# Optimization experiments

Hardware: AMD Instinct MI355X
Metric: run time of the kernel (lower is better)

## Reference

```python
import jax, jax.numpy as jnp
import numpy as np

H = 8          # num_heads
NEG = -1e30    # masked-score value
EPS = 1e-5


def layer_norm(h, g, b):
    mu = jnp.mean(h, -1, keepdims=True)
    v = jnp.mean(jnp.square(h - mu), -1, keepdims=True)
    return (h - mu) * jax.lax.rsqrt(v + EPS) * g + b


def mha(q_in, kv_in, in_w, in_b, out_w, out_b, mask):
    # in_w: [3D, D] packed q/k/v projections (PyTorch MultiheadAttention layout)
    D = q_in.shape[-1]
    dh = D // H
    wq, wk, wv = in_w[:D], in_w[D:2 * D], in_w[2 * D:]
    bq, bk, bv = in_b[:D], in_b[D:2 * D], in_b[2 * D:]
    q = (q_in @ wq.T + bq).reshape(q_in.shape[0], q_in.shape[1], H, dh)
    k = (kv_in @ wk.T + bk).reshape(kv_in.shape[0], kv_in.shape[1], H, dh)
    v = (kv_in @ wv.T + bv).reshape(kv_in.shape[0], kv_in.shape[1], H, dh)
    s = jnp.einsum('bqhd,bkhd->bhqk', q, k) / jnp.sqrt(jnp.float32(dh))
    if mask is not None:
        s = s + mask  # [1,1,S,S] additive causal mask
    a = jax.nn.softmax(s, axis=-1)
    o = jnp.einsum('bhqk,bkhd->bqhd', a, v).reshape(q_in.shape[0], q_in.shape[1], D)
    return o @ out_w.T + out_b


def _forward(x, start_query, one_emb, zero_emb,
             sa_in_w, sa_in_b, sa_out_w, sa_out_b,
             ca_in_w, ca_in_b, ca_out_w, ca_out_b,
             lin1_w, lin1_b, lin2_w, lin2_b,
             ln_g, ln_b, cls_w, cls_b, label):
    B, S, D = x.shape
    n = label.shape[0]  # == S
    # Teacher-forced decoder inputs: [start_query, emb(label[0]), ..., emb(label[n-2])]
    tok = jnp.where((label[:-1] > 0.5)[:, None], one_emb[None, :], zero_emb[None, :])  # [n-1, D]
    tgt = jnp.concatenate([start_query[None, :], tok], axis=0)  # [n, D]
    h = jnp.broadcast_to(tgt[None], (B, n, D))
    causal = jnp.tril(jnp.ones((n, n), dtype=bool))
    mask = jnp.where(causal, 0.0, NEG).astype(x.dtype)[None, None]
    L = sa_in_w.shape[0]
    for l in range(L):
        # post-LN TransformerDecoderLayer (PyTorch default, relu FFN)
        sa = mha(h, h, sa_in_w[l], sa_in_b[l], sa_out_w[l], sa_out_b[l], mask)
        h = layer_norm(h + sa, ln_g[l, 0], ln_b[l, 0])
        ca = mha(h, x, ca_in_w[l], ca_in_b[l], ca_out_w[l], ca_out_b[l], None)
        h = layer_norm(h + ca, ln_g[l, 1], ln_b[l, 1])
        ff = jax.nn.relu(h @ lin1_w[l].T + lin1_b[l]) @ lin2_w[l].T + lin2_b[l]
        h = layer_norm(h + ff, ln_g[l, 2], ln_b[l, 2])
    # classifier + sigmoid; output[b, i] == decoder(tf[:1+i])[-1] of the original loop
    return jax.nn.sigmoid(h @ cls_w.T + cls_b)  # [B, n, 1]


def setup_inputs() -> dict:
    key = jax.random.key(0)
    ks = iter(jax.random.split(key, 32))
    B, S, D, FF, L = 8, 1024, 1024, 2048, 6

    def w(shape, s=0.02):
        return jax.random.normal(next(ks), shape, jnp.float32) * s

    return dict(
        x=jax.random.normal(next(ks), (B, S, D), jnp.float32),
        label=jax.random.uniform(next(ks), (S,), jnp.float32),
        start_query=jax.random.uniform(next(ks), (D,), jnp.float32),
        one_emb=jax.random.uniform(next(ks), (D,), jnp.float32),
        zero_emb=jax.random.uniform(next(ks), (D,), jnp.float32),
        sa_in_w=w((L, 3 * D, D)), sa_in_b=jnp.zeros((L, 3 * D), jnp.float32),
        sa_out_w=w((L, D, D)), sa_out_b=jnp.zeros((L, D), jnp.float32),
        ca_in_w=w((L, 3 * D, D)), ca_in_b=jnp.zeros((L, 3 * D), jnp.float32),
        ca_out_w=w((L, D, D)), ca_out_b=jnp.zeros((L, D), jnp.float32),
        lin1_w=w((L, FF, D)), lin1_b=jnp.zeros((L, FF), jnp.float32),
        lin2_w=w((L, D, FF)), lin2_b=jnp.zeros((L, D), jnp.float32),
        ln_g=jnp.ones((L, 3, D), jnp.float32), ln_b=jnp.zeros((L, 3, D), jnp.float32),
        cls_w=w((1, D)), cls_b=jnp.zeros((1,), jnp.float32),
    )


def reference(x, label, start_query, one_emb, zero_emb,
              sa_in_w, sa_in_b, sa_out_w, sa_out_b,
              ca_in_w, ca_in_b, ca_out_w, ca_out_b,
              lin1_w, lin1_b, lin2_w, lin2_b,
              ln_g, ln_b, cls_w, cls_b):
    return _forward(x, start_query, one_emb, zero_emb,
                    sa_in_w, sa_in_b, sa_out_w, sa_out_b,
                    ca_in_w, ca_in_b, ca_out_w, ca_out_b,
                    lin1_w, lin1_b, lin2_w, lin2_b,
                    ln_g, ln_b, cls_w, cls_b, label)
```

## Files before the change

kernel.cpp:

```cpp
#include <hip/hip_runtime.h>
#include <stdint.h>

typedef __attribute__((ext_vector_type(8))) short short8;
typedef __attribute__((ext_vector_type(4))) float f32x4;
typedef __attribute__((ext_vector_type(4))) float float4v;
typedef __attribute__((ext_vector_type(4))) unsigned short ushort4v;

__device__ __forceinline__ float b2f(short u) {
  union { float f; uint32_t i; } v; v.i = ((uint32_t)(unsigned short)u) << 16; return v.f;
}
__device__ __forceinline__ short f2b(float f) {
  uint32_t x = __float_as_uint(f);
  uint32_t r = (x + 0x7fffu + ((x >> 16) & 1u)) >> 16;
  return (short)r;
}
__device__ __forceinline__ void gload16(const short* g, short* l) {
  __builtin_amdgcn_global_load_lds((__attribute__((address_space(1))) const void*)g,
                                   (__attribute__((address_space(3))) void*)l, 16, 0, 0);
}

__global__ void f2b_kernel(const float* __restrict__ in, short* __restrict__ out, int n4) {
  int i = blockIdx.x * blockDim.x + threadIdx.x;
  int stride = gridDim.x * blockDim.x;
  for (; i < n4; i += stride) {
    float4v v = *((const float4v*)in + i);
    ushort4v o;
    o[0] = (unsigned short)f2b(v[0]); o[1] = (unsigned short)f2b(v[1]);
    o[2] = (unsigned short)f2b(v[2]); o[3] = (unsigned short)f2b(v[3]);
    *((ushort4v*)out + i) = o;
  }
}

__global__ void h0_kernel(const float* __restrict__ label, const float* __restrict__ sq,
                          const float* __restrict__ onee, const float* __restrict__ zeroe,
                          short* __restrict__ h) {
  int i = blockIdx.x;
  const float* src = (i == 0) ? sq : (label[i - 1] > 0.5f ? onee : zeroe);
  int d = threadIdx.x * 4;
  float4v v = *(const float4v*)(src + d);
  ushort4v o;
  o[0] = (unsigned short)f2b(v[0]); o[1] = (unsigned short)f2b(v[1]);
  o[2] = (unsigned short)f2b(v[2]); o[3] = (unsigned short)f2b(v[3]);
#pragma unroll
  for (int b = 0; b < 8; ++b)
    *(ushort4v*)(h + ((size_t)b * 1024 + i) * 1024 + d) = o;
}

__device__ __forceinline__ void stage_grp(const short* __restrict__ mat, size_t rc0,
                                          int K, int kt, short* dstbuf, int w, int lane, int g2) {
  const int w3 = w & 3;
  const int rlo = lane >> 3;
  const int us = (lane & 7) ^ rlo;
#pragma unroll
  for (int q = 0; q < 4; ++q) {
    int c;
    if (w < 4) c = g2 * 8 + w3 * 2 + (q & 1) + (q >> 1) * 16;
    else       c = g2 * 4 + w3 + (q & 1) * 8 + (q >> 1) * 16;
    int rih = (c & 15) * 8 + rlo;
    gload16(mat + (rc0 + (c >> 4) * 128 + rih) * (size_t)K + kt * 64 + us * 8,
            dstbuf + ((w >> 2) * 32 + c) * 512);
  }
}

template <int EPI>
__global__ __launch_bounds__(512, 2) void gemm256(const short* __restrict__ A,
                                                  const short* __restrict__ W,
                                                  const float* __restrict__ bias,
                                                  short* __restrict__ C,
                                                  int M, int N, int K) {
  __shared__ short lds[2 * 4 * 8192];
  const int tid = threadIdx.x, lane = tid & 63, w = tid >> 6;
  const int g = lane >> 4, l15 = lane & 15;
  const int wm = w >> 2, wn = w & 3;
  const int nbx = N >> 8;
  int nwg = gridDim.x, orig = blockIdx.x, cpx = nwg >> 3;
  int id = (orig & 7) * cpx + (orig >> 3);
  int bx = id % nbx, by = id / nbx;
  const size_t rowA = (size_t)by * 256, colB = (size_t)bx * 256;
  const int NT = K >> 6;

  const short* smat = (w < 4) ? A : W;
  const size_t src0 = (w < 4) ? rowA : colB;

  f32x4 acc[8][4];
#pragma unroll
  for (int i = 0; i < 8; ++i)
#pragma unroll
    for (int j = 0; j < 4; ++j) acc[i][j] = (f32x4){0.f, 0.f, 0.f, 0.f};

  int sxz0 = g ^ (l15 & 7);
  int sxz1 = (4 + g) ^ (l15 & 7);
  const short* abase = lds + wm * 8192 + l15 * 64;
  const short* bbase = lds + (2 + (wn >> 1)) * 8192 + ((wn & 1) * 64 + l15) * 64;

  stage_grp(smat, src0, K, 0, lds, w, lane, 0);
  stage_grp(smat, src0, K, 0, lds, w, lane, 1);
  asm volatile("s_waitcnt vmcnt(0)" ::: "memory");
  __builtin_amdgcn_s_barrier();

  int p = 0;
  for (int t = 0; t < NT; ++t) {
    const int po = p * 32768;
    short* nbuf = lds + (p ^ 1) * 32768;
    if (t + 1 < NT) stage_grp(smat, src0, K, t + 1, nbuf, w, lane, 0);
    short8 af[4][2], bf0[2][2], bf1[2][2];

#pragma unroll
    for (int i = 0; i < 4; ++i) {
      af[i][0] = *(const short8*)(abase + po + i * 1024 + sxz0 * 8);
      af[i][1] = *(const short8*)(abase + po + i * 1024 + sxz1 * 8);
    }
#pragma unroll
    for (int j = 0; j < 2; ++j) {
      bf0[j][0] = *(const short8*)(bbase + po + j * 1024 + sxz0 * 8);
      bf0[j][1] = *(const short8*)(bbase + po + j * 1024 + sxz1 * 8);
    }
    __builtin_amdgcn_s_barrier();
    __builtin_amdgcn_s_setprio(1);
#pragma unroll
    for (int i = 0; i < 4; ++i)
#pragma unroll
      for (int j = 0; j < 2; ++j)
#pragma unroll
        for (int ks = 0; ks < 2; ++ks)
          acc[i][j] = __builtin_amdgcn_mfma_f32_16x16x32_bf16(af[i][ks], bf0[j][ks], acc[i][j], 0, 0, 0);
    __builtin_amdgcn_s_setprio(0);
    if (t + 1 < NT) {
      asm volatile("s_waitcnt vmcnt(4)" ::: "memory");
      stage_grp(smat, src0, K, t + 1, nbuf, w, lane, 1);
    } else {
      asm volatile("s_waitcnt vmcnt(0)" ::: "memory");
    }
    __builtin_amdgcn_s_barrier();

#pragma unroll
    for (int j = 0; j < 2; ++j) {
      bf1[j][0] = *(const short8*)(bbase + po + (2 + j) * 1024 + sxz0 * 8);
      bf1[j][1] = *(const short8*)(bbase + po + (2 + j) * 1024 + sxz1 * 8);
    }
    __builtin_amdgcn_s_barrier();
    __builtin_amdgcn_s_setprio(1);
#pragma unroll
    for (int i = 0; i < 4; ++i)
#pragma unroll
      for (int j = 0; j < 2; ++j)
#pragma unroll
        for (int ks = 0; ks < 2; ++ks)
          acc[i][2 + j] = __builtin_amdgcn_mfma_f32_16x16x32_bf16(af[i][ks], bf1[j][ks], acc[i][2 + j], 0, 0, 0);
    __builtin_amdgcn_s_setprio(0);
    __builtin_amdgcn_s_barrier();

#pragma unroll
    for (int i = 0; i < 4; ++i) {
      af[i][0] = *(const short8*)(abase + po + (64 + i * 16) * 64 + sxz0 * 8);
      af[i][1] = *(const short8*)(abase + po + (64 + i * 16) * 64 + sxz1 * 8);
    }
    __builtin_amdgcn_s_barrier();
    __builtin_amdgcn_s_setprio(1);
#pragma unroll
    for (int i = 0; i < 4; ++i)
#pragma unroll
      for (int j = 0; j < 2; ++j)
#pragma unroll
        for (int ks = 0; ks < 2; ++ks)
          acc[4 + i][2 + j] = __builtin_amdgcn_mfma_f32_16x16x32_bf16(af[i][ks], bf1[j][ks], acc[4 + i][2 + j], 0, 0, 0);
    __builtin_amdgcn_s_setprio(0);
    __builtin_amdgcn_s_barrier();

    __builtin_amdgcn_s_setprio(1);
#pragma unroll
    for (int i = 0; i < 4; ++i)
#pragma unroll
      for (int j = 0; j < 2; ++j)
#pragma unroll
        for (int ks = 0; ks < 2; ++ks)
          acc[4 + i][j] = __builtin_amdgcn_mfma_f32_16x16x32_bf16(af[i][ks], bf0[j][ks], acc[4 + i][j], 0, 0, 0);
    __builtin_amdgcn_s_setprio(0);

    asm volatile("s_waitcnt vmcnt(4)" ::: "memory");
    __builtin_amdgcn_s_barrier();
    p ^= 1;
  }

  float bv[4];
#pragma unroll
  for (int j = 0; j < 4; ++j) bv[j] = bias[colB + wn * 64 + j * 16 + l15];
#pragma unroll
  for (int i = 0; i < 8; ++i) {
    size_t row = rowA + wm * 128 + i * 16 + g * 4;
#pragma unroll
    for (int j = 0; j < 4; ++j) {
      size_t col = colB + wn * 64 + j * 16 + l15;
#pragma unroll
      for (int r = 0; r < 4; ++r) {
        float v = acc[i][j][r] + bv[j];
        if (EPI == 1) v = fmaxf(v, 0.f);
        C[(row + r) * N + col] = f2b(v);
      }
    }
  }
}

__device__ __forceinline__ void stage128(const short* __restrict__ A, const short* __restrict__ W,
                                         size_t rowA, size_t colB, int K, int kt,
                                         short* dstbuf, int w, int lane, int grp) {
  const int rlo = lane >> 3;
  const int us = (lane & 7) ^ rlo;
  const int coff = kt * 64 + us * 8;
  if (grp == 0) {
#pragma unroll
    for (int q = 0; q < 4; ++q) {
      int c = w * 4 + q;
      gload16(A + (rowA + c * 8 + rlo) * (size_t)K + coff, dstbuf + c * 512 + lane * 8);
    }
#pragma unroll
    for (int e = 0; e < 2; ++e) {
      int i8 = w * 2 + e;
      int bc = (i8 & 3) + ((i8 >> 2) << 3);
      gload16(W + (colB + bc * 8 + rlo) * (size_t)K + coff, dstbuf + 8192 + bc * 512 + lane * 8);
    }
  } else {
#pragma unroll
    for (int e = 0; e < 2; ++e) {
      int i8 = w * 2 + e;
      int bc = (i8 & 3) + 4 + ((i8 >> 2) << 3);
      gload16(W + (colB + bc * 8 + rlo) * (size_t)K + coff, dstbuf + 8192 + bc * 512 + lane * 8);
    }
  }
}

template <int EPI>
__global__ __launch_bounds__(256, 2) void gemm128(const short* __restrict__ A,
                                                  const short* __restrict__ W,
                                                  const float* __restrict__ bias,
                                                  short* __restrict__ C,
                                                  int M, int N, int K) {
  __shared__ short lds[2 * 16384];
  const int tid = threadIdx.x, lane = tid & 63, w = tid >> 6;
  const int g = lane >> 4, l15 = lane & 15;
  const int wm = w >> 1, wn = w & 1;
  const int nbx = N >> 7;
  int nwg = gridDim.x, orig = blockIdx.x, cpx = nwg >> 3;
  int id = (orig & 7) * cpx + (orig >> 3);
  int bx = id % nbx, by = id / nbx;
  const size_t rowA = (size_t)by * 128, colB = (size_t)bx * 128;
  const int NT = K >> 6;

  f32x4 acc[4][4];
#pragma unroll
  for (int i = 0; i < 4; ++i)
#pragma unroll
    for (int j = 0; j < 4; ++j) acc[i][j] = (f32x4){0.f, 0.f, 0.f, 0.f};

  const int sxz0 = g ^ (l15 & 7), sxz1 = (4 + g) ^ (l15 & 7);

  stage128(A, W, rowA, colB, K, 0, lds, w, lane, 0);
  stage128(A, W, rowA, colB, K, 0, lds, w, lane, 1);
  asm volatile("s_waitcnt vmcnt(0)" ::: "memory");
  __builtin_amdgcn_s_barrier();

  int p = 0;
  for (int t = 0; t < NT; ++t) {
    short* nbuf = lds + (p ^ 1) * 16384;
    if (t + 1 < NT) stage128(A, W, rowA, colB, K, t + 1, nbuf, w, lane, 0);
    const int po = p * 16384;
    short8 af[4][2], bf[2][2];
#pragma unroll
    for (int i = 0; i < 4; ++i) {
      int ra = wm * 64 + i * 16 + l15;
      af[i][0] = *(const short8*)(lds + po + ra * 64 + sxz0 * 8);
      af[i][1] = *(const short8*)(lds + po + ra * 64 + sxz1 * 8);
    }
#pragma unroll
    for (int j = 0; j < 2; ++j) {
      int rb = wn * 64 + j * 16 + l15;
      bf[j][0] = *(const short8*)(lds + po + 8192 + rb * 64 + sxz0 * 8);
      bf[j][1] = *(const short8*)(lds + po + 8192 + rb * 64 + sxz1 * 8);
    }
    __builtin_amdgcn_s_setprio(1);
#pragma unroll
    for (int i = 0; i < 4; ++i)
#pragma unroll
      for (int j = 0; j < 2; ++j)
#pragma unroll
        for (int ks = 0; ks < 2; ++ks)
          acc[i][j] = __builtin_amdgcn_mfma_f32_16x16x32_bf16(af[i][ks], bf[j][ks], acc[i][j], 0, 0, 0);
    __builtin_amdgcn_s_setprio(0);
    if (t + 1 < NT) {
      asm volatile("s_waitcnt vmcnt(6)" ::: "memory");
      stage128(A, W, rowA, colB, K, t + 1, nbuf, w, lane, 1);
    } else {
      asm volatile("s_waitcnt vmcnt(0)" ::: "memory");
    }
    __builtin_amdgcn_s_barrier();
#pragma unroll
    for (int j = 0; j < 2; ++j) {
      int rb = wn * 64 + 32 + j * 16 + l15;
      bf[j][0] = *(const short8*)(lds + po + 8192 + rb * 64 + sxz0 * 8);
      bf[j][1] = *(const short8*)(lds + po + 8192 + rb * 64 + sxz1 * 8);
    }
    __builtin_amdgcn_s_setprio(1);
#pragma unroll
    for (int i = 0; i < 4; ++i)
#pragma unroll
      for (int j = 0; j < 2; ++j)
#pragma unroll
        for (int ks = 0; ks < 2; ++ks)
          acc[i][2 + j] = __builtin_amdgcn_mfma_f32_16x16x32_bf16(af[i][ks], bf[j][ks], acc[i][2 + j], 0, 0, 0);
    __builtin_amdgcn_s_setprio(0);
    asm volatile("s_waitcnt vmcnt(2)" ::: "memory");
    __builtin_amdgcn_s_barrier();
    p ^= 1;
  }

  float bv[4];
#pragma unroll
  for (int j = 0; j < 4; ++j) bv[j] = bias[colB + wn * 64 + j * 16 + l15];
#pragma unroll
  for (int i = 0; i < 4; ++i) {
    size_t row = rowA + wm * 64 + i * 16 + g * 4;
#pragma unroll
    for (int j = 0; j < 4; ++j) {
      size_t col = colB + wn * 64 + j * 16 + l15;
#pragma unroll
      for (int r = 0; r < 4; ++r) {
        float v = acc[i][j][r] + bv[j];
        if (EPI == 1) v = fmaxf(v, 0.f);
        C[(row + r) * N + col] = f2b(v);
      }
    }
  }
}

__global__ __launch_bounds__(256) void tv_kernel(const short* __restrict__ src, int ld, int voff,
                                                 short* __restrict__ vt) {
  __shared__ short t[64 * 72];
  const int kt = blockIdx.x * 64, dt = blockIdx.y * 64, bh = blockIdx.z;
  const int b = bh >> 3, hh = bh & 7;
  const short* s = src + (size_t)(b * 1024 + kt) * ld + voff + hh * 128 + dt;
#pragma unroll
  for (int p = 0; p < 2; ++p) {
    int idx = p * 256 + threadIdx.x;
    int r = idx >> 3, u = idx & 7;
    *(short8*)&t[r * 72 + u * 8] = *(const short8*)&s[(size_t)r * ld + u * 8];
  }
  __syncthreads();
#pragma unroll
  for (int p = 0; p < 2; ++p) {
    int idx = p * 256 + threadIdx.x;
    int dd = idx >> 3, u = idx & 7;
    short8 o;
#pragma unroll
    for (int j = 0; j < 8; ++j) o[j] = t[(u * 8 + j) * 72 + dd];
    *(short8*)&vt[((size_t)bh * 128 + dt + dd) * 1024 + kt + u * 8] = o;
  }
}

template <bool CAUSAL>
__global__ __launch_bounds__(256, 2) void attn_kernel(const short* __restrict__ Qb, int ldq, int qoff,
                                                      const short* __restrict__ Kb, int ldk, int koff,
                                                      const short* __restrict__ Vt,
                                                      short* __restrict__ Ob) {
  __shared__ short k_lds[64 * 128];
  __shared__ short v_lds[128 * 64];
  __shared__ short p_lds[4 * 32 * 72];
  const int tid = threadIdx.x, lane = tid & 63, w = tid >> 6;
  const int g = lane >> 4, l15 = lane & 15;
  const int bh = blockIdx.x, b = bh >> 3, hh = bh & 7;
  const int qi = blockIdx.y;
  const int q0 = qi * 128;
  const float scale = 0.08838834764831845f;
  const int ntiles = CAUSAL ? (q0 >> 6) + 2 : 16;

  const int kr = w * 16 + (lane >> 4);
  const int vd = w * 32 + (lane >> 3);

  short8 qf[2][4];
#pragma unroll
  for (int fm = 0; fm < 2; ++fm) {
    int row = q0 + w * 32 + fm * 16 + l15;
    const short* qp = Qb + (size_t)(b * 1024 + row) * ldq + qoff + hh * 128;
#pragma unroll
    for (int t = 0; t < 4; ++t) qf[fm][t] = *(const short8*)(qp + t * 32 + g * 8);
  }

  f32x4 oacc[2][8];
  f32x4 lacc[2];
  float m_st[2][4];
#pragma unroll
  for (int fm = 0; fm < 2; ++fm) {
#pragma unroll
    for (int fo = 0; fo < 8; ++fo) oacc[fm][fo] = (f32x4){0.f, 0.f, 0.f, 0.f};
    lacc[fm] = (f32x4){0.f, 0.f, 0.f, 0.f};
#pragma unroll
    for (int r = 0; r < 4; ++r) m_st[fm][r] = -3.0e38f;
  }
  const short8 ones = {16256, 16256, 16256, 16256, 16256, 16256, 16256, 16256};

#pragma unroll
  for (int c = 0; c < 4; ++c) {
    int ch = w * 4 + c;
    int r = kr + c * 4;
    int us = (lane & 15) ^ (r & 7);
    gload16(Kb + (size_t)(b * 1024 + r) * ldk + koff + hh * 128 + us * 8, k_lds + ch * 512);
    int d = vd + c * 8;
    int usv = (lane & 7) ^ (d & 7);
    gload16(Vt + ((size_t)bh * 128 + d) * 1024 + usv * 8, v_lds + ch * 512);
  }
  __builtin_amdgcn_sched_barrier(0);
  short8 kreg[4], vreg[4];
  if (ntiles > 1) {
#pragma unroll
    for (int c = 0; c < 4; ++c) {
      int r = kr + c * 4;
      int us = (lane & 15) ^ (r & 7);
      kreg[c] = *(const short8*)(Kb + (size_t)(b * 1024 + 64 + r) * ldk + koff + hh * 128 + us * 8);
      int d = vd + c * 8;
      int usv = (lane & 7) ^ (d & 7);
      vreg[c] = *(const short8*)(Vt + ((size_t)bh * 128 + d) * 1024 + 64 + usv * 8);
    }
    asm volatile("s_waitcnt vmcnt(8)" ::: "memory");
  } else {
    asm volatile("s_waitcnt vmcnt(0)" ::: "memory");
  }
  __builtin_amdgcn_s_barrier();

  for (int kt = 0; kt < ntiles; ++kt) {
    f32x4 sacc[2][4];
#pragma unroll
    for (int fm = 0; fm < 2; ++fm)
#pragma unroll
      for (int fn = 0; fn < 4; ++fn) sacc[fm][fn] = (f32x4){0.f, 0.f, 0.f, 0.f};
#pragma unroll
    for (int t = 0; t < 4; ++t) {
      short8 kf[4];
#pragma unroll
      for (int fn = 0; fn < 4; ++fn) {
        int rowk = fn * 16 + l15;
        int u = (4 * t + g) ^ (rowk & 7);
        kf[fn] = *(const short8*)((const char*)k_lds + rowk * 256 + u * 16);
      }
      __builtin_amdgcn_s_setprio(1);
#pragma unroll
      for (int fm = 0; fm < 2; ++fm)
#pragma unroll
        for (int fn = 0; fn < 4; ++fn)
          sacc[fm][fn] = __builtin_amdgcn_mfma_f32_16x16x32_bf16(qf[fm][t], kf[fn], sacc[fm][fn], 0, 0, 0);
      __builtin_amdgcn_s_setprio(0);
    }

#pragma unroll
    for (int fm = 0; fm < 2; ++fm)
#pragma unroll
      for (int reg = 0; reg < 4; ++reg) {
        float sv[4];
        float mt = -3.0e38f;
#pragma unroll
        for (int fn = 0; fn < 4; ++fn) {
          float s = sacc[fm][fn][reg] * scale;
          if (CAUSAL) {
            int kg = kt * 64 + fn * 16 + l15;
            int qg = q0 + w * 32 + fm * 16 + g * 4 + reg;
            if (kg > qg) s = -1e30f;
          }
          sv[fn] = s;
          mt = fmaxf(mt, s);
        }
#pragma unroll
        for (int off = 1; off < 16; off <<= 1) mt = fmaxf(mt, __shfl_xor(mt, off));
        float mo = m_st[fm][reg];
        float mn = fmaxf(mo, mt);
        float corr = __expf(mo - mn);
#pragma unroll
        for (int fn = 0; fn < 4; ++fn) {
          float p = __expf(sv[fn] - mn);
          p_lds[w * 2304 + (fm * 16 + g * 4 + reg) * 72 + fn * 16 + l15] = f2b(p);
        }
        m_st[fm][reg] = mn;
        lacc[fm][reg] *= corr;
#pragma unroll
        for (int fo = 0; fo < 8; ++fo) oacc[fm][fo][reg] *= corr;
      }

#pragma unroll
    for (int t = 0; t < 2; ++t) {
      short8 pf[2];
#pragma unroll
      for (int fm = 0; fm < 2; ++fm)
        pf[fm] = *(const short8*)(p_lds + w * 2304 + (fm * 16 + l15) * 72 + t * 32 + g * 8);
      __builtin_amdgcn_s_setprio(1);
      lacc[0] = __builtin_amdgcn_mfma_f32_16x16x32_bf16(pf[0], ones, lacc[0], 0, 0, 0);
      lacc[1] = __builtin_amdgcn_mfma_f32_16x16x32_bf16(pf[1], ones, lacc[1], 0, 0, 0);
      __builtin_amdgcn_s_setprio(0);
#pragma unroll
      for (int fo = 0; fo < 8; ++fo) {
        int rowd = fo * 16 + l15;
        int u = (4 * t + g) ^ (rowd & 7);
        short8 vf = *(const short8*)((const char*)v_lds + rowd * 128 + u * 16);
        __builtin_amdgcn_s_setprio(1);
#pragma unroll
        for (int fm = 0; fm < 2; ++fm)
          oacc[fm][fo] = __builtin_amdgcn_mfma_f32_16x16x32_bf16(pf[fm], vf, oacc[fm][fo], 0, 0, 0);
        __builtin_amdgcn_s_setprio(0);
      }
    }

    if (kt + 1 < ntiles) {
      __builtin_amdgcn_s_barrier();
      asm volatile("s_waitcnt vmcnt(0)" ::: "memory");
#pragma unroll
      for (int c = 0; c < 4; ++c) {
        int ch = w * 4 + c;
        *(short8*)(k_lds + ch * 512 + lane * 8) = kreg[c];
        *(short8*)(v_lds + ch * 512 + lane * 8) = vreg[c];
      }
      if (kt + 2 < ntiles) {
#pragma unroll
        for (int c = 0; c < 4; ++c) {
          int r = kr + c * 4;
          int us = (lane & 15) ^ (r & 7);
          kreg[c] = *(const short8*)(Kb + (size_t)(b * 1024 + (kt + 2) * 64 + r) * ldk + koff + hh * 128 + us * 8);
          int d = vd + c * 8;
          int usv = (lane & 7) ^ (d & 7);
          vreg[c] = *(const short8*)(Vt + ((size_t)bh * 128 + d) * 1024 + (kt + 2) * 64 + usv * 8);
        }
      }
      asm volatile("s_waitcnt lgkmcnt(0)" ::: "memory");
      __builtin_amdgcn_s_barrier();
    }
  }

#pragma unroll
  for (int fm = 0; fm < 2; ++fm)
#pragma unroll
    for (int fo = 0; fo < 8; ++fo)
#pragma unroll
      for (int reg = 0; reg < 4; ++reg) {
        int row = q0 + w * 32 + fm * 16 + g * 4 + reg;
        int col = hh * 128 + fo * 16 + l15;
        float o = oacc[fm][fo][reg] / lacc[fm][reg];
        Ob[(size_t)(b * 1024 + row) * 1024 + col] = f2b(o);
      }
}

__global__ __launch_bounds__(128) void ln_kernel(const short* __restrict__ h,
                                                 const short* __restrict__ delta,
                                                 const float* __restrict__ gg,
                                                 const float* __restrict__ bb,
                                                 short* __restrict__ out) {
  __shared__ float red[4];
  const int row = blockIdx.x, tid = threadIdx.x;
  const short8 hv = *(const short8*)(h + (size_t)row * 1024 + tid * 8);
  const short8 dv = *(const short8*)(delta + (size_t)row * 1024 + tid * 8);
  float x[8];
  float s = 0.f, s2 = 0.f;
#pragma unroll
  for (int j = 0; j < 8; ++j) {
    x[j] = b2f(hv[j]) + b2f(dv[j]);
    s += x[j];
    s2 += x[j] * x[j];
  }
#pragma unroll
  for (int o = 1; o < 64; o <<= 1) { s += __shfl_xor(s, o); s2 += __shfl_xor(s2, o); }
  if ((tid & 63) == 0) { red[(tid >> 6) * 2] = s; red[(tid >> 6) * 2 + 1] = s2; }
  __syncthreads();
  s = red[0] + red[2];
  s2 = red[1] + red[3];
  const float mu = s * (1.f / 1024.f);
  const float var = s2 * (1.f / 1024.f) - mu * mu;
  const float rs = rsqrtf(var + 1e-5f);
  short8 o;
#pragma unroll
  for (int j = 0; j < 8; ++j) {
    int d = tid * 8 + j;
    o[j] = f2b((x[j] - mu) * rs * gg[d] + bb[d]);
  }
  *(short8*)(out + (size_t)row * 1024 + tid * 8) = o;
}

__global__ __launch_bounds__(256) void cls_kernel(const short* __restrict__ h,
                                                  const float* __restrict__ wv,
                                                  const float* __restrict__ bias,
                                                  float* __restrict__ out) {
  const int lane = threadIdx.x & 63, w = threadIdx.x >> 6;
  const int row = blockIdx.x * 4 + w;
  const short* hp = h + (size_t)row * 1024 + lane * 16;
  float sum = 0.f;
#pragma unroll
  for (int i = 0; i < 2; ++i) {
    short8 v = *(const short8*)(hp + i * 8);
#pragma unroll
    for (int j = 0; j < 8; ++j) sum += b2f(v[j]) * wv[lane * 16 + i * 8 + j];
  }
#pragma unroll
  for (int o = 1; o < 64; o <<= 1) sum += __shfl_xor(sum, o);
  if (lane == 0) {
    float z = sum + bias[0];
    out[row] = 1.f / (1.f + __expf(-z));
  }
}

#define O_SA_IN  ((size_t)0)
#define O_SA_OUT ((size_t)18874368)
#define O_CA_IN  ((size_t)25165824)
#define O_CA_OUT ((size_t)44040192)
#define O_LIN1   ((size_t)50331648)
#define O_LIN2   ((size_t)62914560)
#define O_X      ((size_t)75497472)
#define O_H      ((size_t)83886080)
#define O_QKV    ((size_t)92274688)
#define O_ATTN   ((size_t)117440512)
#define O_DELTA  ((size_t)125829120)
#define O_VT     ((size_t)134217728)
#define O_FF1    ((size_t)142606336)

extern "C" void kernel_launch(void* const* d_in, const int* in_sizes, int n_in,
                              void* d_out, int out_size, void* d_ws, size_t ws_size,
                              hipStream_t stream) {
  const float* x = (const float*)d_in[0];
  const float* label = (const float*)d_in[1];
  const float* sq = (const float*)d_in[2];
  const float* onee = (const float*)d_in[3];
  const float* zeroe = (const float*)d_in[4];
  const float* sa_in_w = (const float*)d_in[5];
  const float* sa_in_b = (const float*)d_in[6];
  const float* sa_out_w = (const float*)d_in[7];
  const float* sa_out_b = (const float*)d_in[8];
  const float* ca_in_w = (const float*)d_in[9];
  const float* ca_in_b = (const float*)d_in[10];
  const float* ca_out_w = (const float*)d_in[11];
  const float* ca_out_b = (const float*)d_in[12];
  const float* lin1_w = (const float*)d_in[13];
  const float* lin1_b = (const float*)d_in[14];
  const float* lin2_w = (const float*)d_in[15];
  const float* lin2_b = (const float*)d_in[16];
  const float* ln_g = (const float*)d_in[17];
  const float* ln_b = (const float*)d_in[18];
  const float* cls_w = (const float*)d_in[19];
  const float* cls_b = (const float*)d_in[20];

  short* ws = (short*)d_ws;
  short* w_sa_in = ws + O_SA_IN;
  short* w_sa_out = ws + O_SA_OUT;
  short* w_ca_in = ws + O_CA_IN;
  short* w_ca_out = ws + O_CA_OUT;
  short* w_lin1 = ws + O_LIN1;
  short* w_lin2 = ws + O_LIN2;
  short* xb = ws + O_X;
  short* hbuf = ws + O_H;
  short* qkv = ws + O_QKV;
  short* kvb = qkv + 8388608;
  short* attnb = ws + O_ATTN;
  short* delta = ws + O_DELTA;
  short* vt = ws + O_VT;
  short* ff1 = ws + O_FF1;

  f2b_kernel<<<4096, 256, 0, stream>>>(sa_in_w, w_sa_in, 18874368 / 4);
  f2b_kernel<<<4096, 256, 0, stream>>>(sa_out_w, w_sa_out, 6291456 / 4);
  f2b_kernel<<<4096, 256, 0, stream>>>(ca_in_w, w_ca_in, 18874368 / 4);
  f2b_kernel<<<4096, 256, 0, stream>>>(ca_out_w, w_ca_out, 6291456 / 4);
  f2b_kernel<<<4096, 256, 0, stream>>>(lin1_w, w_lin1, 12582912 / 4);
  f2b_kernel<<<4096, 256, 0, stream>>>(lin2_w, w_lin2, 12582912 / 4);
  f2b_kernel<<<4096, 256, 0, stream>>>(x, xb, 8388608 / 4);
  h0_kernel<<<1024, 256, 0, stream>>>(label, sq, onee, zeroe, hbuf);

  for (int l = 0; l < 6; ++l) {
    gemm256<0><<<384, 512, 0, stream>>>(hbuf, w_sa_in + (size_t)l * 3145728,
                                        sa_in_b + (size_t)l * 3072, qkv, 8192, 3072, 1024);
    tv_kernel<<<dim3(16, 2, 64), 256, 0, stream>>>(qkv, 3072, 2048, vt);
    attn_kernel<true><<<dim3(64, 8), 256, 0, stream>>>(qkv, 3072, 0, qkv, 3072, 1024, vt, attnb);
    gemm128<0><<<512, 256, 0, stream>>>(attnb, w_sa_out + (size_t)l * 1048576,
                                        sa_out_b + (size_t)l * 1024, delta, 8192, 1024, 1024);
    ln_kernel<<<8192, 128, 0, stream>>>(hbuf, delta, ln_g + (size_t)(l * 3 + 0) * 1024,
                                        ln_b + (size_t)(l * 3 + 0) * 1024, hbuf);
    gemm128<0><<<512, 256, 0, stream>>>(hbuf, w_ca_in + (size_t)l * 3145728,
                                        ca_in_b + (size_t)l * 3072, qkv, 8192, 1024, 1024);
    gemm256<0><<<256, 512, 0, stream>>>(xb, w_ca_in + (size_t)l * 3145728 + 1048576,
                                        ca_in_b + (size_t)l * 3072 + 1024, kvb, 8192, 2048, 1024);
    tv_kernel<<<dim3(16, 2, 64), 256, 0, stream>>>(kvb, 2048, 1024, vt);
    attn_kernel<false><<<dim3(64, 8), 256, 0, stream>>>(qkv, 1024, 0, kvb, 2048, 0, vt, attnb);
    gemm128<0><<<512, 256, 0, stream>>>(attnb, w_ca_out + (size_t)l * 1048576,
                                        ca_out_b + (size_t)l * 1024, delta, 8192, 1024, 1024);
    ln_kernel<<<8192, 128, 0, stream>>>(hbuf, delta, ln_g + (size_t)(l * 3 + 1) * 1024,
                                        ln_b + (size_t)(l * 3 + 1) * 1024, hbuf);
    gemm256<1><<<256, 512, 0, stream>>>(hbuf, w_lin1 + (size_t)l * 2097152,
                                        lin1_b + (size_t)l * 2048, ff1, 8192, 2048, 1024);
    gemm128<0><<<512, 256, 0, stream>>>(ff1, w_lin2 + (size_t)l * 2097152,
                                        lin2_b + (size_t)l * 1024, delta, 8192, 1024, 2048);
    ln_kernel<<<8192, 128, 0, stream>>>(hbuf, delta, ln_g + (size_t)(l * 3 + 2) * 1024,
                                        ln_b + (size_t)(l * 3 + 2) * 1024, hbuf);
  }
  cls_kernel<<<2048, 256, 0, stream>>>(hbuf, cls_w, cls_b, (float*)d_out);
}
```

Measured before the change: 2.570 ms.

## Split-K output GEMMs with 256 tiles, fold softmax scale into Q projection

The N=1024 output and FFN2 projections now use a split-K 256x256 kernel. Each of the two K halves writes its own bf16 partial, one into the spare vt buffer, and the layer-norm kernel adds both partials to the residual. The attention scale and log2(e) are folded into the Q projection epilogue, so attention can use raw v_exp_f32 (exp2) and a cheaper bf16 round without a per-score multiply. The aim is to raise tile efficiency and occupancy on the small-N GEMMs and to trim softmax ALU work. The cost is an extra partial-sum write and read in the layer norm, plus extra bf16 rounding error from storing the partials.

```diff
diff --git a/kernel.cpp b/kernel.cpp
--- a/kernel.cpp
+++ b/kernel.cpp
@@ -14,10 +14,18 @@
   uint32_t r = (x + 0x7fffu + ((x >> 16) & 1u)) >> 16;
   return (short)r;
 }
+__device__ __forceinline__ short f2b_fast(float f) {
+  return (short)((__float_as_uint(f) + 0x8000u) >> 16);
+}
+__device__ __forceinline__ float exp2_fast(float x) {
+  float r; asm("v_exp_f32 %0, %1" : "=v"(r) : "v"(x)); return r;
+}
 __device__ __forceinline__ void gload16(const short* g, short* l) {
   __builtin_amdgcn_global_load_lds((__attribute__((address_space(1))) const void*)g,
                                    (__attribute__((address_space(3))) void*)l, 16, 0, 0);
 }
+
+#define QSCALE 0.12751744f
 
 __global__ void f2b_kernel(const float* __restrict__ in, short* __restrict__ out, int n4) {
   int i = blockIdx.x * blockDim.x + threadIdx.x;
@@ -62,12 +70,14 @@
   }
 }
 
+
 template <int EPI>
 __global__ __launch_bounds__(512, 2) void gemm256(const short* __restrict__ A,
                                                   const short* __restrict__ W,
                                                   const float* __restrict__ bias,
                                                   short* __restrict__ C,
-                                                  int M, int N, int K) {
+                                                  int M, int N, int K,
+                                                  float qscale, int qcols) {
   __shared__ short lds[2 * 4 * 8192];
   const int tid = threadIdx.x, lane = tid & 63, w = tid >> 6;
   const int g = lane >> 4, l15 = lane & 15;
@@ -191,12 +201,152 @@
 #pragma unroll
     for (int j = 0; j < 4; ++j) {
       size_t col = colB + wn * 64 + j * 16 + l15;
+      float sc = ((int)col < qcols) ? qscale : 1.f;
 #pragma unroll
       for (int r = 0; r < 4; ++r) {
-        float v = acc[i][j][r] + bv[j];
+        float v = (acc[i][j][r] + bv[j]) * sc;
         if (EPI == 1) v = fmaxf(v, 0.f);
         C[(row + r) * N + col] = f2b(v);
       }
+    }
+  }
+}
+
+__global__ __launch_bounds__(512, 2) void gemm256sk(const short* __restrict__ A,
+                                                    const short* __restrict__ W,
+                                                    const float* __restrict__ bias,
+                                                    short* __restrict__ C0,
+                                                    short* __restrict__ C1,
+                                                    int M, int N, int K) {
+  __shared__ short lds[2 * 4 * 8192];
+  const int tid = threadIdx.x, lane = tid & 63, w = tid >> 6;
+  const int g = lane >> 4, l15 = lane & 15;
+  const int wm = w >> 2, wn = w & 3;
+  const int nbx = N >> 8;
+  int nwg = gridDim.x, orig = blockIdx.x, cpx = nwg >> 3;
+  int id = (orig & 7) * cpx + (orig >> 3);
+  int sk = id & 1, tile = id >> 1;
+  int bx = tile % nbx, by = tile / nbx;
+  const size_t rowA = (size_t)by * 256, colB = (size_t)bx * 256;
+  const int NT = K >> 7;
+  const int kb64 = sk * NT;
+
+  const short* smat = (w < 4) ? A : W;
+  const size_t src0 = (w < 4) ? rowA : colB;
+
+  f32x4 acc[8][4];
+#pragma unroll
+  for (int i = 0; i < 8; ++i)
+#pragma unroll
+    for (int j = 0; j < 4; ++j) acc[i][j] = (f32x4){0.f, 0.f, 0.f, 0.f};
+
+  int sxz0 = g ^ (l15 & 7);
+  int sxz1 = (4 + g) ^ (l15 & 7);
+  const short* abase = lds + wm * 8192 + l15 * 64;
+  const short* bbase = lds + (2 + (wn >> 1)) * 8192 + ((wn & 1) * 64 + l15) * 64;
+
+  stage_grp(smat, src0, K, kb64, lds, w, lane, 0);
+  stage_grp(smat, src0, K, kb64, lds, w, lane, 1);
+  asm volatile("s_waitcnt vmcnt(0)" ::: "memory");
+  __builtin_amdgcn_s_barrier();
+
+  int p = 0;
+  for (int t = 0; t < NT; ++t) {
+    const int po = p * 32768;
+    short* nbuf = lds + (p ^ 1) * 32768;
+    if (t + 1 < NT) stage_grp(smat, src0, K, kb64 + t + 1, nbuf, w, lane, 0);
+    short8 af[4][2], bf0[2][2], bf1[2][2];
+
+#pragma unroll
+    for (int i = 0; i < 4; ++i) {
+      af[i][0] = *(const short8*)(abase + po + i * 1024 + sxz0 * 8);
+      af[i][1] = *(const short8*)(abase + po + i * 1024 + sxz1 * 8);
+    }
+#pragma unroll
+    for (int j = 0; j < 2; ++j) {
+      bf0[j][0] = *(const short8*)(bbase + po + j * 1024 + sxz0 * 8);
+      bf0[j][1] = *(const short8*)(bbase + po + j * 1024 + sxz1 * 8);
+    }
+    __builtin_amdgcn_s_barrier();
+    __builtin_amdgcn_s_setprio(1);
+#pragma unroll
+    for (int i = 0; i < 4; ++i)
+#pragma unroll
+      for (int j = 0; j < 2; ++j)
+#pragma unroll
+        for (int ks = 0; ks < 2; ++ks)
+          acc[i][j] = __builtin_amdgcn_mfma_f32_16x16x32_bf16(af[i][ks], bf0[j][ks], acc[i][j], 0, 0, 0);
+    __builtin_amdgcn_s_setprio(0);
+    if (t + 1 < NT) {
+      asm volatile("s_waitcnt vmcnt(4)" ::: "memory");
+      stage_grp(smat, src0, K, kb64 + t + 1, nbuf, w, lane, 1);
+    } else {
+      asm volatile("s_waitcnt vmcnt(0)" ::: "memory");
+    }
+    __builtin_amdgcn_s_barrier();
+
+#pragma unroll
+    for (int j = 0; j < 2; ++j) {
+      bf1[j][0] = *(const short8*)(bbase + po + (2 + j) * 1024 + sxz0 * 8);
+      bf1[j][1] = *(const short8*)(bbase + po + (2 + j) * 1024 + sxz1 * 8);
+    }
+    __builtin_amdgcn_s_barrier();
+    __builtin_amdgcn_s_setprio(1);
+#pragma unroll
+    for (int i = 0; i < 4; ++i)
+#pragma unroll
+      for (int j = 0; j < 2; ++j)
+#pragma unroll
+        for (int ks = 0; ks < 2; ++ks)
+          acc[i][2 + j] = __builtin_amdgcn_mfma_f32_16x16x32_bf16(af[i][ks], bf1[j][ks], acc[i][2 + j], 0, 0, 0);
+    __builtin_amdgcn_s_setprio(0);
+    __builtin_amdgcn_s_barrier();
+
+#pragma unroll
+    for (int i = 0; i < 4; ++i) {
+      af[i][0] = *(const short8*)(abase + po + (64 + i * 16) * 64 + sxz0 * 8);
+      af[i][1] = *(const short8*)(abase + po + (64 + i * 16) * 64 + sxz1 * 8);
+    }
+    __builtin_amdgcn_s_barrier();
+    __builtin_amdgcn_s_setprio(1);
+#pragma unroll
+    for (int i = 0; i < 4; ++i)
+#pragma unroll
+      for (int j = 0; j < 2; ++j)
+#pragma unroll
+        for (int ks = 0; ks < 2; ++ks)
+          acc[4 + i][2 + j] = __builtin_amdgcn_mfma_f32_16x16x32_bf16(af[i][ks], bf1[j][ks], acc[4 + i][2 + j], 0, 0, 0);
+    __builtin_amdgcn_s_setprio(0);
+    __builtin_amdgcn_s_barrier();
+
+    __builtin_amdgcn_s_setprio(1);
+#pragma unroll
+    for (int i = 0; i < 4; ++i)
+#pragma unroll
+      for (int j = 0; j < 2; ++j)
+#pragma unroll
+        for (int ks = 0; ks < 2; ++ks)
+          acc[4 + i][j] = __builtin_amdgcn_mfma_f32_16x16x32_bf16(af[i][ks], bf0[j][ks], acc[4 + i][j], 0, 0, 0);
+    __builtin_amdgcn_s_setprio(0);
+
+    asm volatile("s_waitcnt vmcnt(4)" ::: "memory");
+    __builtin_amdgcn_s_barrier();
+    p ^= 1;
+  }
+
+  short* C = sk ? C1 : C0;
+  float bv[4];
+#pragma unroll
+  for (int j = 0; j < 4; ++j) bv[j] = sk ? 0.f : bias[colB + wn * 64 + j * 16 + l15];
+#pragma unroll
+  for (int i = 0; i < 8; ++i) {
+    size_t row = rowA + wm * 128 + i * 16 + g * 4;
+#pragma unroll
+    for (int j = 0; j < 4; ++j) {
+      size_t col = colB + wn * 64 + j * 16 + l15;
+#pragma unroll
+      for (int r = 0; r < 4; ++r)
+        C[(row + r) * N + col] = f2b(acc[i][j][r] + bv[j]);
     }
   }
 }
@@ -229,12 +379,11 @@
   }
 }
 
-template <int EPI>
 __global__ __launch_bounds__(256, 2) void gemm128(const short* __restrict__ A,
                                                   const short* __restrict__ W,
                                                   const float* __restrict__ bias,
                                                   short* __restrict__ C,
-                                                  int M, int N, int K) {
+                                                  int M, int N, int K, float qscale) {
   __shared__ short lds[2 * 16384];
   const int tid = threadIdx.x, lane = tid & 63, w = tid >> 6;
   const int g = lane >> 4, l15 = lane & 15;
@@ -323,11 +472,8 @@
     for (int j = 0; j < 4; ++j) {
       size_t col = colB + wn * 64 + j * 16 + l15;
 #pragma unroll
-      for (int r = 0; r < 4; ++r) {
-        float v = acc[i][j][r] + bv[j];
-        if (EPI == 1) v = fmaxf(v, 0.f);
-        C[(row + r) * N + col] = f2b(v);
-      }
+      for (int r = 0; r < 4; ++r)
+        C[(row + r) * N + col] = f2b((acc[i][j][r] + bv[j]) * qscale);
     }
   }
 }
@@ -369,7 +515,6 @@
   const int bh = blockIdx.x, b = bh >> 3, hh = bh & 7;
   const int qi = blockIdx.y;
   const int q0 = qi * 128;
-  const float scale = 0.08838834764831845f;
   const int ntiles = CAUSAL ? (q0 >> 6) + 2 : 16;
 
   const int kr = w * 16 + (lane >> 4);
@@ -457,7 +602,7 @@
         float mt = -3.0e38f;
 #pragma unroll
         for (int fn = 0; fn < 4; ++fn) {
-          float s = sacc[fm][fn][reg] * scale;
+          float s = sacc[fm][fn][reg];
           if (CAUSAL) {
             int kg = kt * 64 + fn * 16 + l15;
             int qg = q0 + w * 32 + fm * 16 + g * 4 + reg;
@@ -470,11 +615,11 @@
         for (int off = 1; off < 16; off <<= 1) mt = fmaxf(mt, __shfl_xor(mt, off));
         float mo = m_st[fm][reg];
         float mn = fmaxf(mo, mt);
-        float corr = __expf(mo - mn);
+        float corr = exp2_fast(mo - mn);
 #pragma unroll
         for (int fn = 0; fn < 4; ++fn) {
-          float p = __expf(sv[fn] - mn);
-          p_lds[w * 2304 + (fm * 16 + g * 4 + reg) * 72 + fn * 16 + l15] = f2b(p);
+          float p = exp2_fast(sv[fn] - mn);
+          p_lds[w * 2304 + (fm * 16 + g * 4 + reg) * 72 + fn * 16 + l15] = f2b_fast(p);
         }
         m_st[fm][reg] = mn;
         lacc[fm][reg] *= corr;
@@ -543,20 +688,22 @@
       }
 }
 
-__global__ __launch_bounds__(128) void ln_kernel(const short* __restrict__ h,
-                                                 const short* __restrict__ delta,
-                                                 const float* __restrict__ gg,
-                                                 const float* __restrict__ bb,
-                                                 short* __restrict__ out) {
+__global__ __launch_bounds__(128) void ln2_kernel(const short* __restrict__ h,
+                                                  const short* __restrict__ d0,
+                                                  const short* __restrict__ d1,
+                                                  const float* __restrict__ gg,
+                                                  const float* __restrict__ bb,
+                                                  short* __restrict__ out) {
   __shared__ float red[4];
   const int row = blockIdx.x, tid = threadIdx.x;
   const short8 hv = *(const short8*)(h + (size_t)row * 1024 + tid * 8);
-  const short8 dv = *(const short8*)(delta + (size_t)row * 1024 + tid * 8);
+  const short8 v0 = *(const short8*)(d0 + (size_t)row * 1024 + tid * 8);
+  const short8 v1 = *(const short8*)(d1 + (size_t)row * 1024 + tid * 8);
   float x[8];
   float s = 0.f, s2 = 0.f;
 #pragma unroll
   for (int j = 0; j < 8; ++j) {
-    x[j] = b2f(hv[j]) + b2f(dv[j]);
+    x[j] = b2f(hv[j]) + b2f(v0[j]) + b2f(v1[j]);
     s += x[j];
     s2 += x[j] * x[j];
   }
@@ -666,29 +813,32 @@
 
   for (int l = 0; l < 6; ++l) {
     gemm256<0><<<384, 512, 0, stream>>>(hbuf, w_sa_in + (size_t)l * 3145728,
-                                        sa_in_b + (size_t)l * 3072, qkv, 8192, 3072, 1024);
+                                        sa_in_b + (size_t)l * 3072, qkv, 8192, 3072, 1024,
+                                        QSCALE, 1024);
     tv_kernel<<<dim3(16, 2, 64), 256, 0, stream>>>(qkv, 3072, 2048, vt);
     attn_kernel<true><<<dim3(64, 8), 256, 0, stream>>>(qkv, 3072, 0, qkv, 3072, 1024, vt, attnb);
-    gemm128<0><<<512, 256, 0, stream>>>(attnb, w_sa_out + (size_t)l * 1048576,
-                                        sa_out_b + (size_t)l * 1024, delta, 8192, 1024, 1024);
-    ln_kernel<<<8192, 128, 0, stream>>>(hbuf, delta, ln_g + (size_t)(l * 3 + 0) * 1024,
-                                        ln_b + (size_t)(l * 3 + 0) * 1024, hbuf);
-    gemm128<0><<<512, 256, 0, stream>>>(hbuf, w_ca_in + (size_t)l * 3145728,
-                                        ca_in_b + (size_t)l * 3072, qkv, 8192, 1024, 1024);
+    gemm256sk<<<256, 512, 0, stream>>>(attnb, w_sa_out + (size_t)l * 1048576,
+                                       sa_out_b + (size_t)l * 1024, delta, vt, 8192, 1024, 1024);
+    ln2_kernel<<<8192, 128, 0, stream>>>(hbuf, delta, vt, ln_g + (size_t)(l * 3 + 0) * 1024,
+                                         ln_b + (size_t)(l * 3 + 0) * 1024, hbuf);
+    gemm128<<<512, 256, 0, stream>>>(hbuf, w_ca_in + (size_t)l * 3145728,
+                                     ca_in_b + (size_t)l * 3072, qkv, 8192, 1024, 1024, QSCALE);
     gemm256<0><<<256, 512, 0, stream>>>(xb, w_ca_in + (size_t)l * 3145728 + 1048576,
-                                        ca_in_b + (size_t)l * 3072 + 1024, kvb, 8192, 2048, 1024);
+                                        ca_in_b + (size_t)l * 3072 + 1024, kvb, 8192, 2048, 1024,
+                                        1.f, 0);
     tv_kernel<<<dim3(16, 2, 64), 256, 0, stream>>>(kvb, 2048, 1024, vt);
     attn_kernel<false><<<dim3(64, 8), 256, 0, stream>>>(qkv, 1024, 0, kvb, 2048, 0, vt, attnb);
-    gemm128<0><<<512, 256, 0, stream>>>(attnb, w_ca_out + (size_t)l * 1048576,
-                                        ca_out_b + (size_t)l * 1024, delta, 8192, 1024, 1024);
-    ln_kernel<<<8192, 128, 0, stream>>>(hbuf, delta, ln_g + (size_t)(l * 3 + 1) * 1024,
-                                        ln_b + (size_t)(l * 3 + 1) * 1024, hbuf);
+    gemm256sk<<<256, 512, 0, stream>>>(attnb, w_ca_out + (size_t)l * 1048576,
+                                       ca_out_b + (size_t)l * 1024, delta, vt, 8192, 1024, 1024);
+    ln2_kernel<<<8192, 128, 0, stream>>>(hbuf, delta, vt, ln_g + (size_t)(l * 3 + 1) * 1024,
+                                         ln_b + (size_t)(l * 3 + 1) * 1024, hbuf);
     gemm256<1><<<256, 512, 0, stream>>>(hbuf, w_lin1 + (size_t)l * 2097152,
-                                        lin1_b + (size_t)l * 2048, ff1, 8192, 2048, 1024);
-    gemm128<0><<<512, 256, 0, stream>>>(ff1, w_lin2 + (size_t)l * 2097152,
-                                        lin2_b + (size_t)l * 1024, delta, 8192, 1024, 2048);
-    ln_kernel<<<8192, 128, 0, stream>>>(hbuf, delta, ln_g + (size_t)(l * 3 + 2) * 1024,
-                                        ln_b + (size_t)(l * 3 + 2) * 1024, hbuf);
+                                        lin1_b + (size_t)l * 2048, ff1, 8192, 2048, 1024,
+                                        1.f, 0);
+    gemm256sk<<<256, 512, 0, stream>>>(ff1, w_lin2 + (size_t)l * 2097152,
+                                       lin2_b + (size_t)l * 1024, delta, vt, 8192, 1024, 2048);
+    ln2_kernel<<<8192, 128, 0, stream>>>(hbuf, delta, vt, ln_g + (size_t)(l * 3 + 2) * 1024,
+                                         ln_b + (size_t)(l * 3 + 2) * 1024, hbuf);
   }
   cls_kernel<<<2048, 256, 0, stream>>>(hbuf, cls_w, cls_b, (float*)d_out);
 }
```

New measurement: 2.590 ms. No clear change (+0.8%).
